# Kernel optimization log

Measured on AMD Instinct MI355X. Metric: run time of the kernel, lower is better.

## Reference

```python
import jax, jax.numpy as jnp
import numpy as np

# Cayley-Dickson octonion multiplication tables (from the source module)
SIGN_TABLE = np.array([
    [+1, -1, -1, -1, -1, -1, -1, -1],
    [+1, +1, +1, -1, +1, -1, -1, +1],
    [+1, -1, +1, +1, +1, +1, -1, -1],
    [+1, +1, -1, +1, +1, -1, +1, -1],
    [+1, -1, -1, -1, +1, +1, +1, +1],
    [+1, +1, -1, +1, -1, +1, -1, +1],
    [+1, +1, +1, -1, -1, +1, +1, -1],
    [+1, -1, +1, +1, -1, -1, +1, +1],
], dtype=np.float32)
WEIGHT_IDX = np.array([
    [0, 1, 2, 3, 4, 5, 6, 7],
    [1, 0, 3, 2, 5, 4, 7, 6],
    [2, 3, 0, 1, 6, 7, 4, 5],
    [3, 2, 1, 0, 7, 6, 5, 4],
    [4, 5, 6, 7, 0, 1, 2, 3],
    [5, 4, 7, 6, 1, 0, 3, 2],
    [6, 7, 4, 5, 2, 3, 0, 1],
    [7, 6, 5, 4, 3, 2, 1, 0],
], dtype=np.int32)

B, T, D_IN, D_OUT = 4, 2048, 4096, 4096
K = D_IN // 8   # per-component input dim
N = D_OUT // 8  # per-component output dim


def setup_inputs() -> dict:
    key = jax.random.key(0)
    k1, k2 = jax.random.split(key)
    x = jax.random.normal(k1, (B, T, D_IN), dtype=jnp.float32)
    weight = jax.random.normal(k2, (8, N, K), dtype=jnp.float32) * (1.0 / np.sqrt(K))
    return {"x": x, "weight": weight}


def reference(x, weight):
    """Fused octonion (Cayley-Dickson) linear layer.

    y_i = sum_j sign[i,j] * x_j @ W[widx[i,j]].T
    x components are contiguous chunks of the last dim: x_j = x[..., j*K:(j+1)*K].
    """
    b, t, f = x.shape
    k = f // 8
    xs = x.reshape(b, t, 8, k)                 # [B,T,8,K], component axis j
    Wg = weight[jnp.asarray(WEIGHT_IDX)]        # [8(i),8(j),N,K] gathered weights
    S = jnp.asarray(SIGN_TABLE, dtype=x.dtype)  # [8(i),8(j)]
    # contract over j (component) and k (features); produce [B,T,i,N]
    y = jnp.einsum('ij,btjk,ijnk->btin', S, xs, Wg)
    return y.reshape(b, t, -1)                  # [B,T,8*N]
```

## Files before the change

### kernel.cpp

```cpp
#include <hip/hip_runtime.h>
#include <stdint.h>

typedef __attribute__((ext_vector_type(8))) short bf16x8;
typedef __attribute__((ext_vector_type(4))) float f32x4;

#define D_IN  4096
#define D_OUT 4096
#define KC 512
#define NC 512
#define NT 64

__constant__ float c_sign[64] = {
 +1,-1,-1,-1,-1,-1,-1,-1,
 +1,+1,+1,-1,+1,-1,-1,+1,
 +1,-1,+1,+1,+1,+1,-1,-1,
 +1,+1,-1,+1,+1,-1,+1,-1,
 +1,-1,-1,-1,+1,+1,+1,+1,
 +1,+1,-1,+1,-1,+1,-1,+1,
 +1,+1,+1,-1,-1,+1,+1,-1,
 +1,-1,+1,+1,-1,-1,+1,+1,
};

__device__ inline unsigned int pack2bf16(float a, float b) {
    unsigned int ua = __builtin_bit_cast(unsigned int, a);
    unsigned int ub = __builtin_bit_cast(unsigned int, b);
    ua = (ua + 0x7FFFu + ((ua >> 16) & 1u)) >> 16;
    ub = (ub + 0x7FFFu + ((ub >> 16) & 1u)) >> 16;
    return ua | (ub << 16);
}

typedef __attribute__((address_space(1))) const unsigned int gas_u32;
typedef __attribute__((address_space(3))) unsigned int las_u32;
#define ASYNC16(g, l) __builtin_amdgcn_global_load_lds((gas_u32*)(g), (las_u32*)(l), 16, 0, 0)
#define SBAR0() __builtin_amdgcn_sched_barrier(0)


__global__ __launch_bounds__(256)
void conv_x(const float* __restrict__ in, unsigned short* __restrict__ out, int n8) {
    int i = blockIdx.x * blockDim.x + threadIdx.x;
    if (i >= n8) return;
    const float4 a = ((const float4*)in)[(size_t)i * 2];
    const float4 b = ((const float4*)in)[(size_t)i * 2 + 1];
    uint4 o;
    o.x = pack2bf16(a.x, a.y); o.y = pack2bf16(a.z, a.w);
    o.z = pack2bf16(b.x, b.y); o.w = pack2bf16(b.z, b.w);
    ((uint4*)out)[i] = o;
}

__global__ __launch_bounds__(256)
void conv_w(const float* __restrict__ W, unsigned short* __restrict__ out) {
    int gid = blockIdx.x * blockDim.x + threadIdx.x;
    int row = gid >> 9;
    int c8  = gid & 511;
    int i = row >> 9, n = row & 511;
    int j = c8 >> 6;
    int k = (c8 & 63) << 3;
    float sgn = c_sign[i * 8 + j];
    const float* src = W + ((((i ^ j) * NC + n) * KC) + k);
    float4 a = *(const float4*)(src);
    float4 b = *(const float4*)(src + 4);
    uint4 o;
    o.x = pack2bf16(a.x * sgn, a.y * sgn); o.y = pack2bf16(a.z * sgn, a.w * sgn);
    o.z = pack2bf16(b.x * sgn, b.y * sgn); o.w = pack2bf16(b.z * sgn, b.w * sgn);
    ((uint4*)out)[gid] = o;
}


#define ENDP do { __builtin_amdgcn_s_barrier(); asm volatile("" ::: "memory"); } while (0)

__device__ __forceinline__ void read_a(bf16x8 (&d)[4], const unsigned short* buf,
                                       int mh, int kk, int lane, int wr) {
#pragma unroll
    for (int f = 0; f < 4; ++f) {
        const int r  = wr * 128 + (mh * 4 + f) * 16 + (lane & 15);
        const int ch = (kk * 4 + (lane >> 4)) ^ (r & 7);
        d[f] = *(const bf16x8*)((const char*)buf + r * 128 + (ch << 4));
    }
}

__device__ __forceinline__ void read_b(bf16x8 (&d)[4], const unsigned short* buf,
                                       int kk, int lane, int wc) {
#pragma unroll
    for (int n = 0; n < 4; ++n) {
        const int r  = wc * 64 + n * 16 + (lane & 15);
        const int ch = (kk * 4 + (lane >> 4)) ^ (r & 7);
        d[n] = *(const bf16x8*)((const char*)buf + r * 128 + (ch << 4));
    }
}

__device__ __forceinline__ void mfma16(f32x4 (&acc)[8][4], int mh,
                                       const bf16x8 (&a)[4], const bf16x8 (&b)[4]) {
#pragma unroll
    for (int f = 0; f < 4; ++f)
#pragma unroll
        for (int n = 0; n < 4; ++n)
            acc[mh * 4 + f][n] = __builtin_amdgcn_mfma_f32_16x16x32_bf16(
                a[f], b[n], acc[mh * 4 + f][n], 0, 0, 0);
}

__device__ __forceinline__ void ktile_pipe(
    const unsigned short* Ac, const unsigned short* Bc,
    const unsigned short* An, const unsigned short* Bn,
    unsigned short* stA, unsigned short* stB,
    const unsigned short* gA1, const unsigned short* gB2,
    f32x4 (&acc)[8][4],
    bf16x8 (&aX)[4], bf16x8 (&aY)[4], bf16x8 (&bX)[4], bf16x8 (&bY)[4],
    size_t goff0, size_t goff1, int loff0, int loff1,
    int lane, int wr, int wc)
{
    read_a(aY, Ac, 1, 0, lane, wr);
    ASYNC16(gA1 + goff0, stA + loff0);
    ASYNC16(gA1 + goff1, stA + loff1);
    SBAR0();
    __builtin_amdgcn_s_barrier();
    SBAR0();
    __builtin_amdgcn_s_setprio(1);
    mfma16(acc, 0, aX, bX);
    __builtin_amdgcn_s_setprio(0);
    SBAR0();
    ENDP;
    read_a(aX, Ac, 0, 1, lane, wr);
    read_b(bY, Bc, 1, lane, wc);
    ASYNC16(gA1 + 128 * D_IN + goff0, stA + 8192 + loff0);
    ASYNC16(gA1 + 128 * D_IN + goff1, stA + 8192 + loff1);
    SBAR0();
    __builtin_amdgcn_s_barrier();
    SBAR0();
    __builtin_amdgcn_s_setprio(1);
    mfma16(acc, 1, aY, bX);
    __builtin_amdgcn_s_setprio(0);
    SBAR0();
    ENDP;
    read_a(aY, Ac, 1, 1, lane, wr);
    ASYNC16(gB2 + goff0, stB + loff0);
    ASYNC16(gB2 + goff1, stB + loff1);
    SBAR0();
    __builtin_amdgcn_s_barrier();
    SBAR0();
    __builtin_amdgcn_s_setprio(1);
    mfma16(acc, 0, aX, bY);
    __builtin_amdgcn_s_setprio(0);
    SBAR0();
    asm volatile("s_waitcnt vmcnt(2)");
    ENDP;
    read_a(aX, An, 0, 0, lane, wr);
    read_b(bX, Bn, 0, lane, wc);
    ASYNC16(gB2 + 128 * D_IN + goff0, stB + 8192 + loff0);
    ASYNC16(gB2 + 128 * D_IN + goff1, stB + 8192 + loff1);
    SBAR0();
    __builtin_amdgcn_s_barrier();
    SBAR0();
    __builtin_amdgcn_s_setprio(1);
    mfma16(acc, 1, aY, bY);
    __builtin_amdgcn_s_setprio(0);
    SBAR0();
    ENDP;
}

__global__ __launch_bounds__(512, 2)
void octo_gemm_8ph(const unsigned short* __restrict__ Xb,
                   const unsigned short* __restrict__ Wb,
                   float* __restrict__ Y, int M)
{
    __shared__ __align__(16) unsigned short sm[65536];
    unsigned short* A0 = sm;
    unsigned short* A1 = sm + 16384;
    unsigned short* B0 = sm + 32768;
    unsigned short* B1 = sm + 49152;

    const int tid  = threadIdx.x;
    const int lane = tid & 63;
    const int wave = tid >> 6;
    const int wr   = wave >> 2;
    const int wc   = wave & 3;

    const int nbn = D_OUT / 256;
    const int nwg = (M / 256) * nbn;
    int bid = blockIdx.x;
    int cpx = nwg >> 3;
    int wg  = (bid & 7) * cpx + (bid >> 3);
    const int bm = wg / nbn, bn = wg % nbn;
    const int row0 = bm * 256, col0 = bn * 256;

    const int srow  = tid >> 3;
    const int sch   = tid & 7;
    const size_t goff0 = (size_t)srow * D_IN + (size_t)((sch ^ (srow & 7)) * 8);
    const size_t goff1 = goff0 + (size_t)64 * D_IN;
    const int loff0 = tid * 8;
    const int loff1 = loff0 + 4096;

    const unsigned short* gX = Xb + (size_t)row0 * D_IN;
    const unsigned short* gW = Wb + (size_t)col0 * D_IN;

    f32x4 acc[8][4];
    #pragma unroll
    for (int m = 0; m < 8; ++m)
        #pragma unroll
        for (int n = 0; n < 4; ++n)
            acc[m][n] = (f32x4){0.f, 0.f, 0.f, 0.f};

    ASYNC16(gX + goff0, A0 + loff0);              ASYNC16(gX + goff1, A0 + loff1);
    ASYNC16(gX + 128 * D_IN + goff0, A0 + 8192 + loff0);
    ASYNC16(gX + 128 * D_IN + goff1, A0 + 8192 + loff1);
    ASYNC16(gW + goff0, B0 + loff0);              ASYNC16(gW + goff1, B0 + loff1);
    ASYNC16(gW + 128 * D_IN + goff0, B0 + 8192 + loff0);
    ASYNC16(gW + 128 * D_IN + goff1, B0 + 8192 + loff1);
    ASYNC16(gW + 64 + goff0, B1 + loff0);         ASYNC16(gW + 64 + goff1, B1 + loff1);
    ASYNC16(gW + 64 + 128 * D_IN + goff0, B1 + 8192 + loff0);
    ASYNC16(gW + 64 + 128 * D_IN + goff1, B1 + 8192 + loff1);
    asm volatile("s_waitcnt vmcnt(4)");
    ENDP;

    bf16x8 aX[4], aY[4], bX[4], bY[4];
    read_a(aX, A0, 0, 0, lane, wr);
    read_b(bX, B0, 0, lane, wc);

    for (int i = 0; i < NT / 2; ++i) {
        const int u = 2 * i;
        const unsigned short* gA1t = gX + ((u + 1) & (NT - 1)) * 64;
        const unsigned short* gA2t = gX + ((u + 2) & (NT - 1)) * 64;
        const unsigned short* gB2t = gW + ((u + 2) & (NT - 1)) * 64;
        const unsigned short* gB3t = gW + ((u + 3) & (NT - 1)) * 64;

        ktile_pipe(A0, B0, A1, B1, A1, B0, gA1t, gB2t,
                   acc, aX, aY, bX, bY,
                   goff0, goff1, loff0, loff1, lane, wr, wc);
        ktile_pipe(A1, B1, A0, B0, A0, B1, gA2t, gB3t,
                   acc, aX, aY, bX, bY,
                   goff0, goff1, loff0, loff1, lane, wr, wc);
    }

    const int rl = (lane >> 4) << 2;
    const int cl = lane & 15;
    #pragma unroll
    for (int m = 0; m < 8; ++m) {
        const int rg = row0 + wr * 128 + m * 16 + rl;
        #pragma unroll
        for (int n = 0; n < 4; ++n) {
            const int cg = col0 + wc * 64 + n * 16 + cl;
            #pragma unroll
            for (int q = 0; q < 4; ++q)
                Y[(size_t)(rg + q) * D_OUT + cg] = acc[m][n][q];
        }
    }
}


#define BM 128
#define BN 128
#define BK 64

__global__ __launch_bounds__(256)
void octo_gemm_f32(const float* __restrict__ X, const float* __restrict__ W,
                   float* __restrict__ Y, int M)
{
    __shared__ __align__(16) unsigned short As[BM * BK];
    __shared__ __align__(16) unsigned short Bs[BN * BK];

    const int tid  = threadIdx.x;
    const int lane = tid & 63;
    const int wave = tid >> 6;
    const int wr   = wave >> 1;
    const int wc   = wave & 1;

    const int nbn = D_OUT / BN;
    const int nwg = (M / BM) * nbn;
    int bid = blockIdx.x;
    int wg  = bid;
    if ((nwg & 7) == 0) {
        int cpx = nwg >> 3;
        wg = (bid & 7) * cpx + (bid >> 3);
    }
    const int bm = wg / nbn, bn = wg % nbn;
    const int row0  = bm * BM;
    const int col0  = bn * BN;
    const int icomp = col0 >> 9;
    const int noff  = col0 & (NC - 1);

    const int srow = tid >> 4;
    const int scol = (tid & 15) << 2;

    f32x4 acc[4][4];
    #pragma unroll
    for (int m = 0; m < 4; ++m)
        #pragma unroll
        for (int n = 0; n < 4; ++n)
            acc[m][n] = (f32x4){0.f, 0.f, 0.f, 0.f};

    char* AsB = (char*)As;
    char* BsB = (char*)Bs;
    const int byteC = scol << 1;

    for (int step = 0; step < NT; ++step) {
        const int k0 = step * BK;
        const int j  = k0 >> 9;
        const int kc = k0 & (KC - 1);
        const float sgn = c_sign[icomp * 8 + j];
        const int   w   = icomp ^ j;
        const float* Wp = W + (((size_t)w * NC + noff) * KC + kc);
        const float* Xp = X + ((size_t)row0 * D_IN + k0);

        __syncthreads();
        #pragma unroll
        for (int p = 0; p < 8; ++p) {
            const int r  = p * 16 + srow;
            const int sb = r * 128 + ((((byteC >> 4) ^ (r & 7)) << 4)) + (byteC & 8);
            const float4 va = *(const float4*)(&Xp[(size_t)r * D_IN + scol]);
            *(uint2*)(AsB + sb) = make_uint2(pack2bf16(va.x, va.y),
                                             pack2bf16(va.z, va.w));
            const float4 vb = *(const float4*)(&Wp[(size_t)r * KC + scol]);
            *(uint2*)(BsB + sb) = make_uint2(pack2bf16(vb.x * sgn, vb.y * sgn),
                                             pack2bf16(vb.z * sgn, vb.w * sgn));
        }
        __syncthreads();

        #pragma unroll
        for (int kk = 0; kk < 2; ++kk) {
            bf16x8 af[4], bf[4];
            #pragma unroll
            for (int m = 0; m < 4; ++m) {
                const int r = wr * 64 + m * 16 + (lane & 15);
                const int chunk = (kk * 4 + (lane >> 4)) ^ (r & 7);
                af[m] = *(const bf16x8*)(AsB + r * 128 + (chunk << 4));
            }
            #pragma unroll
            for (int n = 0; n < 4; ++n) {
                const int r = wc * 64 + n * 16 + (lane & 15);
                const int chunk = (kk * 4 + (lane >> 4)) ^ (r & 7);
                bf[n] = *(const bf16x8*)(BsB + r * 128 + (chunk << 4));
            }
            #pragma unroll
            for (int m = 0; m < 4; ++m)
                #pragma unroll
                for (int n = 0; n < 4; ++n)
                    acc[m][n] = __builtin_amdgcn_mfma_f32_16x16x32_bf16(
                        af[m], bf[n], acc[m][n], 0, 0, 0);
        }
    }

    const int rl = (lane >> 4) << 2;
    const int cl = lane & 15;
    #pragma unroll
    for (int m = 0; m < 4; ++m) {
        const int rg = row0 + wr * 64 + m * 16 + rl;
        #pragma unroll
        for (int n = 0; n < 4; ++n) {
            const int cg = col0 + wc * 64 + n * 16 + cl;
            #pragma unroll
            for (int q = 0; q < 4; ++q)
                Y[(size_t)(rg + q) * D_OUT + cg] = acc[m][n][q];
        }
    }
}

extern "C" void kernel_launch(void* const* d_in, const int* in_sizes, int n_in,
                              void* d_out, int out_size, void* d_ws, size_t ws_size,
                              hipStream_t stream) {
    const float* X = (const float*)d_in[0];
    const float* W = (const float*)d_in[1];
    float* Y = (float*)d_out;
    const int M = in_sizes[0] / D_IN;

    const size_t xb_bytes = (size_t)M * D_IN * sizeof(unsigned short);
    const size_t wb_bytes = (size_t)D_OUT * D_IN * sizeof(unsigned short);

    if (ws_size >= xb_bytes + wb_bytes && (M % 256) == 0) {
        unsigned short* Xb = (unsigned short*)d_ws;
        unsigned short* Wb = (unsigned short*)((char*)d_ws + xb_bytes);
        const int n8x = M * D_IN / 8;
        hipLaunchKernelGGL(conv_x, dim3(n8x / 256), dim3(256), 0, stream, X, Xb, n8x);
        hipLaunchKernelGGL(conv_w, dim3((D_OUT * D_IN / 8) / 256), dim3(256), 0, stream, W, Wb);
        const int nwg = (M / 256) * (D_OUT / 256);
        hipLaunchKernelGGL(octo_gemm_8ph, dim3(nwg), dim3(512), 0, stream, Xb, Wb, Y, M);
    } else {
        const int nwg = (M / BM) * (D_OUT / BN);
        hipLaunchKernelGGL(octo_gemm_f32, dim3(nwg), dim3(256), 0, stream, X, W, Y, M);
    }
}
```

Measured before the change: 262.4 us.

## Load B operand straight from global into registers, drop B LDS staging

```diff
diff --git a/kernel.cpp b/kernel.cpp
--- a/kernel.cpp
+++ b/kernel.cpp
@@ -33,6 +33,7 @@
 typedef __attribute__((address_space(3))) unsigned int las_u32;
 #define ASYNC16(g, l) __builtin_amdgcn_global_load_lds((gas_u32*)(g), (las_u32*)(l), 16, 0, 0)
 #define SBAR0() __builtin_amdgcn_sched_barrier(0)
+#define ENDP do { __builtin_amdgcn_s_barrier(); asm volatile("" ::: "memory"); } while (0)
 
 
 __global__ __launch_bounds__(256)
@@ -66,8 +67,6 @@
 }
 
 
-#define ENDP do { __builtin_amdgcn_s_barrier(); asm volatile("" ::: "memory"); } while (0)
-
 __device__ __forceinline__ void read_a(bf16x8 (&d)[4], const unsigned short* buf,
                                        int mh, int kk, int lane, int wr) {
 #pragma unroll
@@ -78,14 +77,11 @@
     }
 }
 
-__device__ __forceinline__ void read_b(bf16x8 (&d)[4], const unsigned short* buf,
-                                       int kk, int lane, int wc) {
-#pragma unroll
-    for (int n = 0; n < 4; ++n) {
-        const int r  = wc * 64 + n * 16 + (lane & 15);
-        const int ch = (kk * 4 + (lane >> 4)) ^ (r & 7);
-        d[n] = *(const bf16x8*)((const char*)buf + r * 128 + (ch << 4));
-    }
+__device__ __forceinline__ bf16x8 gload_b(const unsigned short* gB, int n, int kk,
+                                          int lane, int wc) {
+    const size_t off = (size_t)(wc * 64 + n * 16 + (lane & 15)) * D_IN
+                     + kk * 32 + (lane >> 4) * 8;
+    return *(const bf16x8*)(gB + off);
 }
 
 __device__ __forceinline__ void mfma16(f32x4 (&acc)[8][4], int mh,
@@ -98,62 +94,66 @@
                 a[f], b[n], acc[mh * 4 + f][n], 0, 0, 0);
 }
 
-__device__ __forceinline__ void ktile_pipe(
-    const unsigned short* Ac, const unsigned short* Bc,
-    const unsigned short* An, const unsigned short* Bn,
-    unsigned short* stA, unsigned short* stB,
-    const unsigned short* gA1, const unsigned short* gB2,
+__device__ __forceinline__ void tile_bg(
+    const unsigned short* Acur, unsigned short* Aoth,
+    const unsigned short* gA1, const unsigned short* gB1,
     f32x4 (&acc)[8][4],
-    bf16x8 (&aX)[4], bf16x8 (&aY)[4], bf16x8 (&bX)[4], bf16x8 (&bY)[4],
+    bf16x8 (&bc0)[4], bf16x8 (&bc1)[4],
+    bf16x8 (&bn0)[4], bf16x8 (&bn1)[4],
     size_t goff0, size_t goff1, int loff0, int loff1,
     int lane, int wr, int wc)
 {
-    read_a(aY, Ac, 1, 0, lane, wr);
-    ASYNC16(gA1 + goff0, stA + loff0);
-    ASYNC16(gA1 + goff1, stA + loff1);
+    bf16x8 a[4];
+    read_a(a, Acur, 0, 0, lane, wr);
+    ASYNC16(gA1 + goff0, Aoth + loff0);
+    ASYNC16(gA1 + goff1, Aoth + loff1);
+    SBAR0();
+    bn0[0] = gload_b(gB1, 0, 0, lane, wc);
+    bn0[1] = gload_b(gB1, 1, 0, lane, wc);
     SBAR0();
     __builtin_amdgcn_s_barrier();
     SBAR0();
     __builtin_amdgcn_s_setprio(1);
-    mfma16(acc, 0, aX, bX);
+    mfma16(acc, 0, a, bc0);
     __builtin_amdgcn_s_setprio(0);
     SBAR0();
     ENDP;
-    read_a(aX, Ac, 0, 1, lane, wr);
-    read_b(bY, Bc, 1, lane, wc);
-    ASYNC16(gA1 + 128 * D_IN + goff0, stA + 8192 + loff0);
-    ASYNC16(gA1 + 128 * D_IN + goff1, stA + 8192 + loff1);
+    read_a(a, Acur, 1, 0, lane, wr);
+    ASYNC16(gA1 + 128 * D_IN + goff0, Aoth + 8192 + loff0);
+    ASYNC16(gA1 + 128 * D_IN + goff1, Aoth + 8192 + loff1);
+    SBAR0();
+    bn0[2] = gload_b(gB1, 2, 0, lane, wc);
+    bn0[3] = gload_b(gB1, 3, 0, lane, wc);
     SBAR0();
     __builtin_amdgcn_s_barrier();
     SBAR0();
     __builtin_amdgcn_s_setprio(1);
-    mfma16(acc, 1, aY, bX);
+    mfma16(acc, 1, a, bc0);
     __builtin_amdgcn_s_setprio(0);
     SBAR0();
     ENDP;
-    read_a(aY, Ac, 1, 1, lane, wr);
-    ASYNC16(gB2 + goff0, stB + loff0);
-    ASYNC16(gB2 + goff1, stB + loff1);
+    read_a(a, Acur, 0, 1, lane, wr);
+    bn1[0] = gload_b(gB1, 0, 1, lane, wc);
+    bn1[1] = gload_b(gB1, 1, 1, lane, wc);
     SBAR0();
     __builtin_amdgcn_s_barrier();
     SBAR0();
     __builtin_amdgcn_s_setprio(1);
-    mfma16(acc, 0, aX, bY);
+    mfma16(acc, 0, a, bc1);
     __builtin_amdgcn_s_setprio(0);
     SBAR0();
-    asm volatile("s_waitcnt vmcnt(2)");
-    ENDP;
-    read_a(aX, An, 0, 0, lane, wr);
-    read_b(bX, Bn, 0, lane, wc);
-    ASYNC16(gB2 + 128 * D_IN + goff0, stB + 8192 + loff0);
-    ASYNC16(gB2 + 128 * D_IN + goff1, stB + 8192 + loff1);
+    ENDP;
+    read_a(a, Acur, 1, 1, lane, wr);
+    bn1[2] = gload_b(gB1, 2, 1, lane, wc);
+    bn1[3] = gload_b(gB1, 3, 1, lane, wc);
     SBAR0();
     __builtin_amdgcn_s_barrier();
     SBAR0();
     __builtin_amdgcn_s_setprio(1);
-    mfma16(acc, 1, aY, bY);
+    mfma16(acc, 1, a, bc1);
     __builtin_amdgcn_s_setprio(0);
     SBAR0();
+    asm volatile("s_waitcnt vmcnt(6)");
     ENDP;
 }
 
@@ -162,11 +162,9 @@
                    const unsigned short* __restrict__ Wb,
                    float* __restrict__ Y, int M)
 {
-    __shared__ __align__(16) unsigned short sm[65536];
+    __shared__ __align__(16) unsigned short sm[32768];
     unsigned short* A0 = sm;
     unsigned short* A1 = sm + 16384;
-    unsigned short* B0 = sm + 32768;
-    unsigned short* B1 = sm + 49152;
 
     const int tid  = threadIdx.x;
     const int lane = tid & 63;
@@ -199,35 +197,35 @@
         for (int n = 0; n < 4; ++n)
             acc[m][n] = (f32x4){0.f, 0.f, 0.f, 0.f};
 
-    ASYNC16(gX + goff0, A0 + loff0);              ASYNC16(gX + goff1, A0 + loff1);
+    ASYNC16(gX + goff0, A0 + loff0);
+    ASYNC16(gX + goff1, A0 + loff1);
     ASYNC16(gX + 128 * D_IN + goff0, A0 + 8192 + loff0);
     ASYNC16(gX + 128 * D_IN + goff1, A0 + 8192 + loff1);
-    ASYNC16(gW + goff0, B0 + loff0);              ASYNC16(gW + goff1, B0 + loff1);
-    ASYNC16(gW + 128 * D_IN + goff0, B0 + 8192 + loff0);
-    ASYNC16(gW + 128 * D_IN + goff1, B0 + 8192 + loff1);
-    ASYNC16(gW + 64 + goff0, B1 + loff0);         ASYNC16(gW + 64 + goff1, B1 + loff1);
-    ASYNC16(gW + 64 + 128 * D_IN + goff0, B1 + 8192 + loff0);
-    ASYNC16(gW + 64 + 128 * D_IN + goff1, B1 + 8192 + loff1);
-    asm volatile("s_waitcnt vmcnt(4)");
-    ENDP;
-
-    bf16x8 aX[4], aY[4], bX[4], bY[4];
-    read_a(aX, A0, 0, 0, lane, wr);
-    read_b(bX, B0, 0, lane, wc);
+    SBAR0();
+    bf16x8 bA0[4], bA1[4], bB0[4], bB1[4];
+    bA0[0] = gload_b(gW, 0, 0, lane, wc);
+    bA0[1] = gload_b(gW, 1, 0, lane, wc);
+    bA0[2] = gload_b(gW, 2, 0, lane, wc);
+    bA0[3] = gload_b(gW, 3, 0, lane, wc);
+    bA1[0] = gload_b(gW, 0, 1, lane, wc);
+    bA1[1] = gload_b(gW, 1, 1, lane, wc);
+    bA1[2] = gload_b(gW, 2, 1, lane, wc);
+    bA1[3] = gload_b(gW, 3, 1, lane, wc);
+    SBAR0();
+    asm volatile("s_waitcnt vmcnt(8)");
+    ENDP;
 
     for (int i = 0; i < NT / 2; ++i) {
         const int u = 2 * i;
         const unsigned short* gA1t = gX + ((u + 1) & (NT - 1)) * 64;
+        const unsigned short* gB1t = gW + ((u + 1) & (NT - 1)) * 64;
         const unsigned short* gA2t = gX + ((u + 2) & (NT - 1)) * 64;
         const unsigned short* gB2t = gW + ((u + 2) & (NT - 1)) * 64;
-        const unsigned short* gB3t = gW + ((u + 3) & (NT - 1)) * 64;
-
-        ktile_pipe(A0, B0, A1, B1, A1, B0, gA1t, gB2t,
-                   acc, aX, aY, bX, bY,
-                   goff0, goff1, loff0, loff1, lane, wr, wc);
-        ktile_pipe(A1, B1, A0, B0, A0, B1, gA2t, gB3t,
-                   acc, aX, aY, bX, bY,
-                   goff0, goff1, loff0, loff1, lane, wr, wc);
+
+        tile_bg(A0, A1, gA1t, gB1t, acc, bA0, bA1, bB0, bB1,
+                goff0, goff1, loff0, loff1, lane, wr, wc);
+        tile_bg(A1, A0, gA2t, gB2t, acc, bB0, bB1, bA0, bA1,
+                goff0, goff1, loff0, loff1, lane, wr, wc);
     }
 
     const int rl = (lane >> 4) << 2;
```

Result: slower. 379.7 us (+44.7%).
